# Performance work log

Measured on AMD Instinct MI355X. Metric: run time of the kernel, lower is better.

## Reference

```python
import jax, jax.numpy as jnp
import numpy as np

B, T, D, K = 8, 4096, 1024, 3


def setup_inputs() -> dict:
    key = jax.random.key(0)
    k0, k1, k2 = jax.random.split(key, 3)
    x = jax.random.normal(k0, (B, T, D), dtype=jnp.float32)
    lim = 1.0 / np.sqrt(D)
    Wv = jax.random.uniform(k1, (D, D), dtype=jnp.float32, minval=-lim, maxval=lim)
    bv = jnp.zeros((D,), dtype=jnp.float32)
    Wo = jax.random.uniform(k2, (D, D), dtype=jnp.float32, minval=-lim, maxval=lim)
    bo = jnp.zeros((D,), dtype=jnp.float32)
    neighbor_weights = jnp.ones((K,), dtype=jnp.float32) / K
    return {"x": x, "Wv": Wv, "bv": bv, "Wo": Wo, "bo": bo,
            "neighbor_weights": neighbor_weights}


def reference(x, Wv, bv, Wo, bo, neighbor_weights):
    # x: [B, T, D]; faithful translation of the unfold -> Linear -> weighted-sum chain
    k = neighbor_weights.shape[0]
    pad = k // 2
    t = x.shape[1]
    # replicate padding along T (torch F.pad mode='replicate')
    xp = jnp.pad(x, ((0, 0), (pad, pad), (0, 0)), mode='edge')  # [B, T+2*pad, D]
    # sliding windows: [B, T, K, D] (small fixed K loop, not a data-dim loop)
    windows = jnp.stack([xp[:, i:i + t, :] for i in range(k)], axis=2)
    # value projection applied per window element (nn.Linear: x @ W.T + b)
    v = jnp.einsum('btkd,ed->btke', windows, Wv) + bv  # [B, T, K, D]
    # fixed-weight neighbor average
    attended = jnp.einsum('btkd,k->btd', v, neighbor_weights)  # [B, T, D]
    # output projection
    return jnp.einsum('btd,ed->bte', attended, Wo) + bo
```

## Files before the change

kernel.cpp:

```cpp
#include <hip/hip_runtime.h>
#include <stdint.h>
#include <stddef.h>

typedef _Float16 f16_t;
typedef _Float16 f16x4 __attribute__((ext_vector_type(4)));
typedef _Float16 f16x8 __attribute__((ext_vector_type(8)));
typedef float f32x4 __attribute__((ext_vector_type(4)));

#define AS_G __attribute__((address_space(1)))
#define AS_L __attribute__((address_space(3)))

__device__ __forceinline__ void gload_lds16(const void* g, void* l) {
  __builtin_amdgcn_global_load_lds((AS_G void*)g, (AS_L void*)l, 16, 0, 0);
}

#define FENCE() asm volatile("" ::: "memory")
#define BARX()                            \
  do {                                    \
    FENCE();                              \
    __builtin_amdgcn_s_barrier();         \
    FENCE();                              \
  } while (0)
#define VMCNT(n) asm volatile("s_waitcnt vmcnt(" #n ")" ::: "memory")


__global__ __launch_bounds__(256) void prep_xavg_kernel(
    const float* __restrict__ X, const float* __restrict__ Wo,
    const float* __restrict__ Wv, const float* __restrict__ bv,
    const float* __restrict__ bo, const float* __restrict__ nw, int Kw,
    f16_t* __restrict__ Wo_h, f16_t* __restrict__ WvT, float* __restrict__ bc,
    f16_t* __restrict__ Xavg) {
  __shared__ float smem[32 * 33];
  const int b = blockIdx.x;
  const int t = threadIdx.x;
  if (b >= 3072) {
    const int T = 4096, D = 1024;
    const int base = (b - 3072) * 8;
    const int t0 = base & (T - 1);
    const int col = t * 4;
    const float w0 = nw[0], w1 = nw[1], w2 = nw[2];
    const float* xb = X + (size_t)base * D + col;
    f32x4 va = *(const f32x4*)(xb + (t0 == 0 ? 0 : -D));
    f32x4 vb = *(const f32x4*)(xb);
    f16_t* ob = Xavg + (size_t)base * D + col;
#pragma unroll
    for (int g = 0; g < 8; ++g) {
      f32x4 vc;
      if (t0 + g == T - 1) vc = vb;
      else vc = *(const f32x4*)(xb + (size_t)(g + 1) * D);
      f32x4 y = w0 * va + w1 * vb + w2 * vc;
      f16x4 o;
      o.x = (f16_t)y.x; o.y = (f16_t)y.y; o.z = (f16_t)y.z; o.w = (f16_t)y.w;
      *(f16x4*)(ob + (size_t)g * D) = o;
      va = vb;
      vb = vc;
    }
  } else if (b < 1024) {
    const int i = b * 256 + t;
    f32x4 v = ((const f32x4*)Wo)[i];
    f16x4 o;
    o.x = (f16_t)v.x; o.y = (f16_t)v.y; o.z = (f16_t)v.z; o.w = (f16_t)v.w;
    ((f16x4*)Wo_h)[i] = o;
  } else if (b < 2048) {
    const int i = b - 1024;
    const int bx = i & 31, by = i >> 5;
    const int tx = t & 31, ty = t >> 5;
#pragma unroll
    for (int k = 0; k < 32; k += 8)
      smem[(ty + k) * 33 + tx] = Wv[(size_t)(by * 32 + ty + k) * 1024 + bx * 32 + tx];
    __syncthreads();
#pragma unroll
    for (int k = 0; k < 32; k += 8)
      WvT[(size_t)(bx * 32 + ty + k) * 1024 + by * 32 + tx] = (f16_t)smem[tx * 33 + ty + k];
  } else {
    const int e = b - 2048;
    float sw = 0.f;
    for (int k = 0; k < Kw; ++k) sw += nw[k];
    float p = 0.f;
    for (int d = t; d < 1024; d += 256) p += Wo[(size_t)e * 1024 + d] * bv[d];
    smem[t] = p;
    __syncthreads();
    for (int s = 128; s > 0; s >>= 1) {
      if (t < s) smem[t] += smem[t + s];
      __syncthreads();
    }
    if (t == 0) bc[e] = sw * smem[0] + bo[e];
  }
}


template <typename OutT, bool BIAS>
__global__ __launch_bounds__(256) void gemm_bt_kernel(const f16_t* __restrict__ A,
                                                      const f16_t* __restrict__ Bt,
                                                      OutT* __restrict__ C,
                                                      const float* __restrict__ bias,
                                                      int M, int N, int K) {
  __shared__ __align__(16) f16_t sA[128 * 32];
  __shared__ __align__(16) f16_t sB[128 * 32];
  const int tid = threadIdx.x;
  const int l = tid & 63;
  const int w = tid >> 6;
  const int wr = w >> 1;
  const int wc = w & 1;
  const int nMT = M >> 7;
  const int bid = blockIdx.x;
  const int mt = bid % nMT;
  const int nt = bid / nMT;
  const int m0 = mt << 7;
  const int n0 = nt << 7;

  const int srow = (w << 4) + (l >> 2);
  const int scol = (l & 3) << 3;
  const size_t aoff0 = (size_t)(m0 + srow) * K + scol;
  const size_t boff0 = (size_t)(n0 + srow) * K + scol;
  f16_t* ldsA = sA + (w << 9);
  f16_t* ldsB = sB + (w << 9);

  f32x4 acc[4][4];
#pragma unroll
  for (int i = 0; i < 4; ++i)
#pragma unroll
    for (int j = 0; j < 4; ++j) acc[i][j] = f32x4{0.f, 0.f, 0.f, 0.f};

  const int ka = (l >> 4) << 3;
  const int ar = (wr << 6) + (l & 15);
  const int br = (wc << 6) + (l & 15);

  const int nK = K >> 5;
  for (int kt = 0; kt < nK; ++kt) {
    const int kb = kt << 5;
    gload_lds16(A + aoff0 + kb, ldsA);
    gload_lds16(A + aoff0 + ((size_t)K << 6) + kb, ldsA + 2048);
    gload_lds16(Bt + boff0 + kb, ldsB);
    gload_lds16(Bt + boff0 + ((size_t)K << 6) + kb, ldsB + 2048);
    __syncthreads();
    f16x8 af[4], bfr[4];
#pragma unroll
    for (int m = 0; m < 4; ++m) af[m] = *(const f16x8*)(sA + ((ar + (m << 4)) << 5) + ka);
#pragma unroll
    for (int n = 0; n < 4; ++n) bfr[n] = *(const f16x8*)(sB + ((br + (n << 4)) << 5) + ka);
#pragma unroll
    for (int m = 0; m < 4; ++m)
#pragma unroll
      for (int n = 0; n < 4; ++n)
        acc[m][n] = __builtin_amdgcn_mfma_f32_16x16x32_f16(af[m], bfr[n], acc[m][n], 0, 0, 0);
    __syncthreads();
  }

  const int orow = (l >> 4) << 2;
  const int ocol = l & 15;
#pragma unroll
  for (int n = 0; n < 4; ++n) {
    const int gn = n0 + (wc << 6) + (n << 4) + ocol;
    const float bs = BIAS ? bias[gn] : 0.f;
#pragma unroll
    for (int m = 0; m < 4; ++m) {
      const int gm = m0 + (wr << 6) + (m << 4) + orow;
#pragma unroll
      for (int j = 0; j < 4; ++j) {
        C[(size_t)(gm + j) * N + gn] = (OutT)(acc[m][n][j] + bs);
      }
    }
  }
}


__device__ __forceinline__ void stage256(const f16_t* __restrict__ g, int K,
                                         f16_t* ldsOp, int w, int l) {
#pragma unroll
  for (int i = 0; i < 2; ++i) {
    const int f = i * 512 + w * 64 + l;
    const int row = f >> 2;
    const int ch = f & 3;
    const int col = ((ch ^ ((row >> 1) & 3)) << 3);
    gload_lds16(g + (size_t)row * K + col, ldsOp + i * 4096 + w * 512);
  }
}

__global__ __launch_bounds__(512, 2) void gemm256_kernel(const f16_t* __restrict__ A,
                                                         const f16_t* __restrict__ Bt,
                                                         float* __restrict__ C,
                                                         const float* __restrict__ bias,
                                                         int M, int N, int K) {
  __shared__ __align__(16) f16_t lds[4 * 16384];
  const int tid = threadIdx.x;
  const int l = tid & 63;
  const int w = tid >> 6;
  const int wr = w >> 2;
  const int wc = w & 3;
  const int lr = l & 15;
  const int q = l >> 4;

  const int cpx = (int)gridDim.x >> 3;
  const int swzb = ((int)blockIdx.x & 7) * cpx + ((int)blockIdx.x >> 3);
  const int nNT = N >> 8;
  const int mt = swzb / nNT;
  const int nt = swzb % nNT;
  const int m0 = mt << 8;
  const int n0 = nt << 8;

  const f16_t* Apanel = A + (size_t)m0 * K;
  const f16_t* Bpanel = Bt + (size_t)n0 * K;
  const int sw = (q ^ ((lr >> 1) & 3)) << 3;

  f32x4 acc[8][4];
#pragma unroll
  for (int m = 0; m < 8; ++m)
#pragma unroll
    for (int n = 0; n < 4; ++n) acc[m][n] = f32x4{0.f, 0.f, 0.f, 0.f};

  const int nK = K >> 5;

  for (int t = 0; t < 3; ++t) {
    f16_t* buf = lds + (t & 3) * 16384;
    stage256(Apanel + (t << 5), K, buf, w, l);
    stage256(Bpanel + (t << 5), K, buf + 8192, w, l);
  }
  VMCNT(8);
  BARX();

  for (int t = 0; t < nK; ++t) {
    f16_t* sA = lds + (t & 3) * 16384;
    f16_t* sB = sA + 8192;

    {
      const int tn = (t + 3) < nK ? (t + 3) : (nK - 1);
      f16_t* nbuf = lds + ((t + 3) & 3) * 16384;
      stage256(Apanel + ((size_t)tn << 5), K, nbuf, w, l);
      stage256(Bpanel + ((size_t)tn << 5), K, nbuf + 8192, w, l);
    }

    f16x8 bf[4], af[4], ag[4];
#pragma unroll
    for (int n = 0; n < 4; ++n)
      bf[n] = *(const f16x8*)(sB + (((wc << 6) + (n << 4) + lr) << 5) + sw);
#pragma unroll
    for (int m = 0; m < 4; ++m)
      af[m] = *(const f16x8*)(sA + (((wr << 7) + (m << 4) + lr) << 5) + sw);
#pragma unroll
    for (int m = 0; m < 4; ++m)
      ag[m] = *(const f16x8*)(sA + (((wr << 7) + 64 + (m << 4) + lr) << 5) + sw);

    __builtin_amdgcn_s_setprio(1);
#pragma unroll
    for (int m = 0; m < 4; ++m)
#pragma unroll
      for (int n = 0; n < 4; ++n)
        acc[m][n] = __builtin_amdgcn_mfma_f32_16x16x32_f16(af[m], bf[n], acc[m][n], 0, 0, 0);
#pragma unroll
    for (int m = 0; m < 4; ++m)
#pragma unroll
      for (int n = 0; n < 4; ++n)
        acc[m + 4][n] = __builtin_amdgcn_mfma_f32_16x16x32_f16(ag[m], bf[n], acc[m + 4][n], 0, 0, 0);
    __builtin_amdgcn_s_setprio(0);

    VMCNT(8);
    BARX();
  }

  float bs[4];
#pragma unroll
  for (int n = 0; n < 4; ++n) bs[n] = bias[n0 + (wc << 6) + (n << 4) + lr];
#pragma unroll
  for (int m = 0; m < 8; ++m) {
    const int gm = m0 + (wr << 7) + (m << 4) + (q << 2);
#pragma unroll
    for (int j = 0; j < 4; ++j) {
      float* Crow = C + (size_t)(gm + j) * N + n0 + (wc << 6) + lr;
#pragma unroll
      for (int n = 0; n < 4; ++n) Crow[n << 4] = acc[m][n][j] + bs[n];
    }
  }
}


extern "C" void kernel_launch(void* const* d_in, const int* in_sizes, int n_in,
                              void* d_out, int out_size, void* d_ws, size_t ws_size,
                              hipStream_t stream) {
  const float* x = (const float*)d_in[0];
  const float* Wv = (const float*)d_in[1];
  const float* bv = (const float*)d_in[2];
  const float* Wo = (const float*)d_in[3];
  const float* bo = (const float*)d_in[4];
  const float* nw = (const float*)d_in[5];
  float* out = (float*)d_out;

  char* ws = (char*)d_ws;
  f16_t* Wo_h = (f16_t*)(ws);
  f16_t* WvT  = (f16_t*)(ws + (2u << 20));
  f16_t* WcT  = (f16_t*)(ws + (4u << 20));
  float* bc   = (float*)(ws + (6u << 20));
  f16_t* Xavg = (f16_t*)(ws + (8u << 20));

  prep_xavg_kernel<<<dim3(7168), dim3(256), 0, stream>>>(
      x, Wo, Wv, bv, bo, nw, in_sizes[5], Wo_h, WvT, bc, Xavg);
  gemm_bt_kernel<f16_t, false><<<dim3(64), dim3(256), 0, stream>>>(
      Wo_h, WvT, WcT, (const float*)nullptr, 1024, 1024, 1024);
  gemm256_kernel<<<dim3(512), dim3(512), 0, stream>>>(
      Xavg, WcT, out, bc, 32768, 1024, 1024);
}
```

Measured before the change: 146.8 us.

## Shrink main GEMM tile to 256x128 with 3-stage LDS pipeline for higher occupancy

```diff
diff --git a/kernel.cpp b/kernel.cpp
--- a/kernel.cpp
+++ b/kernel.cpp
@@ -165,24 +165,24 @@
 }
 
 
-__device__ __forceinline__ void stage256(const f16_t* __restrict__ g, int K,
-                                         f16_t* ldsOp, int w, int l) {
+__device__ __forceinline__ void stageOp(const f16_t* __restrict__ g, int K, int rows2,
+                                        f16_t* gran, int w, int l) {
 #pragma unroll
   for (int i = 0; i < 2; ++i) {
+    if (i >= rows2) break;
     const int f = i * 512 + w * 64 + l;
     const int row = f >> 2;
-    const int ch = f & 3;
-    const int col = ((ch ^ ((row >> 1) & 3)) << 3);
-    gload_lds16(g + (size_t)row * K + col, ldsOp + i * 4096 + w * 512);
-  }
-}
-
-__global__ __launch_bounds__(512, 2) void gemm256_kernel(const f16_t* __restrict__ A,
+    const int ch = (f & 3) ^ ((row >> 1) & 3);
+    gload_lds16(g + (size_t)row * K + (ch << 3), gran + i * 4096 + w * 512);
+  }
+}
+
+__global__ __launch_bounds__(512, 4) void gemm_hi_kernel(const f16_t* __restrict__ A,
                                                          const f16_t* __restrict__ Bt,
                                                          float* __restrict__ C,
                                                          const float* __restrict__ bias,
                                                          int M, int N, int K) {
-  __shared__ __align__(16) f16_t lds[4 * 16384];
+  __shared__ __align__(16) f16_t lds[3 * 12288];
   const int tid = threadIdx.x;
   const int l = tid & 63;
   const int w = tid >> 6;
@@ -193,82 +193,77 @@
 
   const int cpx = (int)gridDim.x >> 3;
   const int swzb = ((int)blockIdx.x & 7) * cpx + ((int)blockIdx.x >> 3);
-  const int nNT = N >> 8;
+  const int nNT = N >> 7;
   const int mt = swzb / nNT;
   const int nt = swzb % nNT;
   const int m0 = mt << 8;
-  const int n0 = nt << 8;
+  const int n0 = nt << 7;
 
   const f16_t* Apanel = A + (size_t)m0 * K;
   const f16_t* Bpanel = Bt + (size_t)n0 * K;
   const int sw = (q ^ ((lr >> 1) & 3)) << 3;
 
-  f32x4 acc[8][4];
+  f32x4 acc[8][2];
 #pragma unroll
   for (int m = 0; m < 8; ++m)
 #pragma unroll
-    for (int n = 0; n < 4; ++n) acc[m][n] = f32x4{0.f, 0.f, 0.f, 0.f};
+    for (int n = 0; n < 2; ++n) acc[m][n] = f32x4{0.f, 0.f, 0.f, 0.f};
 
   const int nK = K >> 5;
 
-  for (int t = 0; t < 3; ++t) {
-    f16_t* buf = lds + (t & 3) * 16384;
-    stage256(Apanel + (t << 5), K, buf, w, l);
-    stage256(Bpanel + (t << 5), K, buf + 8192, w, l);
-  }
-  VMCNT(8);
+#define STAGE(TT, GI)                                                       \
+  do {                                                                      \
+    const int ts_ = (TT) < nK ? (TT) : (nK - 1);                            \
+    f16_t* g_ = lds + (GI) * 12288;                                         \
+    stageOp(Apanel + (ts_ << 5), K, 2, g_, w, l);                           \
+    stageOp(Bpanel + (ts_ << 5), K, 1, g_ + 8192, w, l);                    \
+  } while (0)
+
+  STAGE(0, 0);
+  STAGE(1, 1);
+  VMCNT(3);
   BARX();
 
+  int cur = 0, stg = 2;
   for (int t = 0; t < nK; ++t) {
-    f16_t* sA = lds + (t & 3) * 16384;
-    f16_t* sB = sA + 8192;
-
-    {
-      const int tn = (t + 3) < nK ? (t + 3) : (nK - 1);
-      f16_t* nbuf = lds + ((t + 3) & 3) * 16384;
-      stage256(Apanel + ((size_t)tn << 5), K, nbuf, w, l);
-      stage256(Bpanel + ((size_t)tn << 5), K, nbuf + 8192, w, l);
-    }
-
-    f16x8 bf[4], af[4], ag[4];
-#pragma unroll
-    for (int n = 0; n < 4; ++n)
-      bf[n] = *(const f16x8*)(sB + (((wc << 6) + (n << 4) + lr) << 5) + sw);
-#pragma unroll
-    for (int m = 0; m < 4; ++m)
-      af[m] = *(const f16x8*)(sA + (((wr << 7) + (m << 4) + lr) << 5) + sw);
-#pragma unroll
-    for (int m = 0; m < 4; ++m)
-      ag[m] = *(const f16x8*)(sA + (((wr << 7) + 64 + (m << 4) + lr) << 5) + sw);
+    STAGE(t + 2, stg);
+
+    const f16_t* gA = lds + cur * 12288;
+    const f16_t* gB = gA + 8192;
+    f16x8 af[8], bf[2];
+#pragma unroll
+    for (int n = 0; n < 2; ++n)
+      bf[n] = *(const f16x8*)(gB + (((wc << 5) + (n << 4) + lr) << 5) + sw);
+#pragma unroll
+    for (int m = 0; m < 8; ++m)
+      af[m] = *(const f16x8*)(gA + (((wr << 7) + (m << 4) + lr) << 5) + sw);
 
     __builtin_amdgcn_s_setprio(1);
 #pragma unroll
-    for (int m = 0; m < 4; ++m)
-#pragma unroll
-      for (int n = 0; n < 4; ++n)
+    for (int m = 0; m < 8; ++m)
+#pragma unroll
+      for (int n = 0; n < 2; ++n)
         acc[m][n] = __builtin_amdgcn_mfma_f32_16x16x32_f16(af[m], bf[n], acc[m][n], 0, 0, 0);
-#pragma unroll
-    for (int m = 0; m < 4; ++m)
-#pragma unroll
-      for (int n = 0; n < 4; ++n)
-        acc[m + 4][n] = __builtin_amdgcn_mfma_f32_16x16x32_f16(ag[m], bf[n], acc[m + 4][n], 0, 0, 0);
     __builtin_amdgcn_s_setprio(0);
 
-    VMCNT(8);
+    VMCNT(3);
     BARX();
-  }
-
-  float bs[4];
-#pragma unroll
-  for (int n = 0; n < 4; ++n) bs[n] = bias[n0 + (wc << 6) + (n << 4) + lr];
+    cur = (cur == 2) ? 0 : cur + 1;
+    stg = (stg == 2) ? 0 : stg + 1;
+  }
+#undef STAGE
+
+  float bs[2];
+#pragma unroll
+  for (int n = 0; n < 2; ++n) bs[n] = bias[n0 + (wc << 5) + (n << 4) + lr];
 #pragma unroll
   for (int m = 0; m < 8; ++m) {
     const int gm = m0 + (wr << 7) + (m << 4) + (q << 2);
 #pragma unroll
     for (int j = 0; j < 4; ++j) {
-      float* Crow = C + (size_t)(gm + j) * N + n0 + (wc << 6) + lr;
-#pragma unroll
-      for (int n = 0; n < 4; ++n) Crow[n << 4] = acc[m][n][j] + bs[n];
+      float* Crow = C + (size_t)(gm + j) * N + n0 + (wc << 5) + lr;
+#pragma unroll
+      for (int n = 0; n < 2; ++n) Crow[n << 4] = acc[m][n][j] + bs[n];
     }
   }
 }
@@ -296,6 +291,6 @@
       x, Wo, Wv, bv, bo, nw, in_sizes[5], Wo_h, WvT, bc, Xavg);
   gemm_bt_kernel<f16_t, false><<<dim3(64), dim3(256), 0, stream>>>(
       Wo_h, WvT, WcT, (const float*)nullptr, 1024, 1024, 1024);
-  gemm256_kernel<<<dim3(512), dim3(512), 0, stream>>>(
+  gemm_hi_kernel<<<dim3(1024), dim3(512), 0, stream>>>(
       Xavg, WcT, out, bc, 32768, 1024, 1024);
 }
```

Result: no change. 147.7 us (+0.7%).

## Overlap X-averaging pass with the weight-combine GEMM in one launch

Applied to the files above, without the earlier changes.

```diff
diff --git a/kernel.cpp b/kernel.cpp
--- a/kernel.cpp
+++ b/kernel.cpp
@@ -24,38 +24,15 @@
 #define VMCNT(n) asm volatile("s_waitcnt vmcnt(" #n ")" ::: "memory")
 
 
-__global__ __launch_bounds__(256) void prep_xavg_kernel(
-    const float* __restrict__ X, const float* __restrict__ Wo,
-    const float* __restrict__ Wv, const float* __restrict__ bv,
-    const float* __restrict__ bo, const float* __restrict__ nw, int Kw,
-    f16_t* __restrict__ Wo_h, f16_t* __restrict__ WvT, float* __restrict__ bc,
-    f16_t* __restrict__ Xavg) {
+__global__ __launch_bounds__(256) void prep_w_kernel(
+    const float* __restrict__ Wo, const float* __restrict__ Wv,
+    const float* __restrict__ bv, const float* __restrict__ bo,
+    const float* __restrict__ nw, int Kw,
+    f16_t* __restrict__ Wo_h, f16_t* __restrict__ WvT, float* __restrict__ bc) {
   __shared__ float smem[32 * 33];
   const int b = blockIdx.x;
   const int t = threadIdx.x;
-  if (b >= 3072) {
-    const int T = 4096, D = 1024;
-    const int base = (b - 3072) * 8;
-    const int t0 = base & (T - 1);
-    const int col = t * 4;
-    const float w0 = nw[0], w1 = nw[1], w2 = nw[2];
-    const float* xb = X + (size_t)base * D + col;
-    f32x4 va = *(const f32x4*)(xb + (t0 == 0 ? 0 : -D));
-    f32x4 vb = *(const f32x4*)(xb);
-    f16_t* ob = Xavg + (size_t)base * D + col;
-#pragma unroll
-    for (int g = 0; g < 8; ++g) {
-      f32x4 vc;
-      if (t0 + g == T - 1) vc = vb;
-      else vc = *(const f32x4*)(xb + (size_t)(g + 1) * D);
-      f32x4 y = w0 * va + w1 * vb + w2 * vc;
-      f16x4 o;
-      o.x = (f16_t)y.x; o.y = (f16_t)y.y; o.z = (f16_t)y.z; o.w = (f16_t)y.w;
-      *(f16x4*)(ob + (size_t)g * D) = o;
-      va = vb;
-      vb = vc;
-    }
-  } else if (b < 1024) {
+  if (b < 1024) {
     const int i = b * 256 + t;
     f32x4 v = ((const f32x4*)Wo)[i];
     f16x4 o;
@@ -89,23 +66,49 @@
 }
 
 
-template <typename OutT, bool BIAS>
-__global__ __launch_bounds__(256) void gemm_bt_kernel(const f16_t* __restrict__ A,
-                                                      const f16_t* __restrict__ Bt,
-                                                      OutT* __restrict__ C,
-                                                      const float* __restrict__ bias,
-                                                      int M, int N, int K) {
-  __shared__ __align__(16) f16_t sA[128 * 32];
-  __shared__ __align__(16) f16_t sB[128 * 32];
+__global__ __launch_bounds__(256) void xavg_wct_kernel(
+    const float* __restrict__ X, const float* __restrict__ nw,
+    const f16_t* __restrict__ Wo_h, const f16_t* __restrict__ WvT,
+    f16_t* __restrict__ Xavg, f16_t* __restrict__ WcT) {
+  __shared__ __align__(16) f16_t smem[2 * 128 * 32];
+  const int b = blockIdx.x;
   const int tid = threadIdx.x;
+
+  if (b < 4096) {
+    const int T = 4096, D = 1024;
+    const int base = b * 8;
+    const int t0 = base & (T - 1);
+    const int col = tid * 4;
+    const float w0 = nw[0], w1 = nw[1], w2 = nw[2];
+    const float* xb = X + (size_t)base * D + col;
+    f32x4 va = *(const f32x4*)(xb + (t0 == 0 ? 0 : -D));
+    f32x4 vb = *(const f32x4*)(xb);
+    f16_t* ob = Xavg + (size_t)base * D + col;
+#pragma unroll
+    for (int g = 0; g < 8; ++g) {
+      f32x4 vc;
+      if (t0 + g == T - 1) vc = vb;
+      else vc = *(const f32x4*)(xb + (size_t)(g + 1) * D);
+      f32x4 y = w0 * va + w1 * vb + w2 * vc;
+      f16x4 o;
+      o.x = (f16_t)y.x; o.y = (f16_t)y.y; o.z = (f16_t)y.z; o.w = (f16_t)y.w;
+      *(f16x4*)(ob + (size_t)g * D) = o;
+      va = vb;
+      vb = vc;
+    }
+    return;
+  }
+
+  constexpr int K = 1024, N = 1024;
+  f16_t* sA = smem;
+  f16_t* sB = smem + 128 * 32;
   const int l = tid & 63;
   const int w = tid >> 6;
   const int wr = w >> 1;
   const int wc = w & 1;
-  const int nMT = M >> 7;
-  const int bid = blockIdx.x;
-  const int mt = bid % nMT;
-  const int nt = bid / nMT;
+  const int bid = b - 4096;
+  const int mt = bid & 7;
+  const int nt = bid >> 3;
   const int m0 = mt << 7;
   const int n0 = nt << 7;
 
@@ -126,13 +129,12 @@
   const int ar = (wr << 6) + (l & 15);
   const int br = (wc << 6) + (l & 15);
 
-  const int nK = K >> 5;
-  for (int kt = 0; kt < nK; ++kt) {
+  for (int kt = 0; kt < (K >> 5); ++kt) {
     const int kb = kt << 5;
-    gload_lds16(A + aoff0 + kb, ldsA);
-    gload_lds16(A + aoff0 + ((size_t)K << 6) + kb, ldsA + 2048);
-    gload_lds16(Bt + boff0 + kb, ldsB);
-    gload_lds16(Bt + boff0 + ((size_t)K << 6) + kb, ldsB + 2048);
+    gload_lds16(Wo_h + aoff0 + kb, ldsA);
+    gload_lds16(Wo_h + aoff0 + ((size_t)K << 6) + kb, ldsA + 2048);
+    gload_lds16(WvT + boff0 + kb, ldsB);
+    gload_lds16(WvT + boff0 + ((size_t)K << 6) + kb, ldsB + 2048);
     __syncthreads();
     f16x8 af[4], bfr[4];
 #pragma unroll
@@ -152,13 +154,12 @@
 #pragma unroll
   for (int n = 0; n < 4; ++n) {
     const int gn = n0 + (wc << 6) + (n << 4) + ocol;
-    const float bs = BIAS ? bias[gn] : 0.f;
 #pragma unroll
     for (int m = 0; m < 4; ++m) {
       const int gm = m0 + (wr << 6) + (m << 4) + orow;
 #pragma unroll
       for (int j = 0; j < 4; ++j) {
-        C[(size_t)(gm + j) * N + gn] = (OutT)(acc[m][n][j] + bs);
+        WcT[(size_t)(gm + j) * N + gn] = (f16_t)acc[m][n][j];
       }
     }
   }
@@ -172,7 +173,7 @@
     const int f = i * 512 + w * 64 + l;
     const int row = f >> 2;
     const int ch = f & 3;
-    const int col = ((ch ^ ((row >> 1) & 3)) << 3);
+    const int col = (((ch ^ ((row >> 1) & 3))) << 3);
     gload_lds16(g + (size_t)row * K + col, ldsOp + i * 4096 + w * 512);
   }
 }
@@ -292,10 +293,10 @@
   float* bc   = (float*)(ws + (6u << 20));
   f16_t* Xavg = (f16_t*)(ws + (8u << 20));
 
-  prep_xavg_kernel<<<dim3(7168), dim3(256), 0, stream>>>(
-      x, Wo, Wv, bv, bo, nw, in_sizes[5], Wo_h, WvT, bc, Xavg);
-  gemm_bt_kernel<f16_t, false><<<dim3(64), dim3(256), 0, stream>>>(
-      Wo_h, WvT, WcT, (const float*)nullptr, 1024, 1024, 1024);
+  prep_w_kernel<<<dim3(3072), dim3(256), 0, stream>>>(
+      Wo, Wv, bv, bo, nw, in_sizes[5], Wo_h, WvT, bc);
+  xavg_wct_kernel<<<dim3(4160), dim3(256), 0, stream>>>(
+      x, nw, Wo_h, WvT, Xavg, WcT);
   gemm256_kernel<<<dim3(512), dim3(512), 0, stream>>>(
       Xavg, WcT, out, bc, 32768, 1024, 1024);
 }
```

Result: no change. 145.1 us (-1.2%).

## Fuse neighbor averaging into main GEMM epilogue, reading fp32 x directly

Applied to the files above, without the earlier changes.

```diff
diff --git a/kernel.cpp b/kernel.cpp
--- a/kernel.cpp
+++ b/kernel.cpp
@@ -6,6 +6,7 @@
 typedef _Float16 f16x4 __attribute__((ext_vector_type(4)));
 typedef _Float16 f16x8 __attribute__((ext_vector_type(8)));
 typedef float f32x4 __attribute__((ext_vector_type(4)));
+typedef float f32x8 __attribute__((ext_vector_type(8)));
 
 #define AS_G __attribute__((address_space(1)))
 #define AS_L __attribute__((address_space(3)))
@@ -24,38 +25,15 @@
 #define VMCNT(n) asm volatile("s_waitcnt vmcnt(" #n ")" ::: "memory")
 
 
-__global__ __launch_bounds__(256) void prep_xavg_kernel(
-    const float* __restrict__ X, const float* __restrict__ Wo,
-    const float* __restrict__ Wv, const float* __restrict__ bv,
-    const float* __restrict__ bo, const float* __restrict__ nw, int Kw,
-    f16_t* __restrict__ Wo_h, f16_t* __restrict__ WvT, float* __restrict__ bc,
-    f16_t* __restrict__ Xavg) {
+__global__ __launch_bounds__(256) void prep_w_kernel(
+    const float* __restrict__ Wo, const float* __restrict__ Wv,
+    const float* __restrict__ bv, const float* __restrict__ bo,
+    const float* __restrict__ nw, int Kw,
+    f16_t* __restrict__ Wo_h, f16_t* __restrict__ WvT, float* __restrict__ bc) {
   __shared__ float smem[32 * 33];
   const int b = blockIdx.x;
   const int t = threadIdx.x;
-  if (b >= 3072) {
-    const int T = 4096, D = 1024;
-    const int base = (b - 3072) * 8;
-    const int t0 = base & (T - 1);
-    const int col = t * 4;
-    const float w0 = nw[0], w1 = nw[1], w2 = nw[2];
-    const float* xb = X + (size_t)base * D + col;
-    f32x4 va = *(const f32x4*)(xb + (t0 == 0 ? 0 : -D));
-    f32x4 vb = *(const f32x4*)(xb);
-    f16_t* ob = Xavg + (size_t)base * D + col;
-#pragma unroll
-    for (int g = 0; g < 8; ++g) {
-      f32x4 vc;
-      if (t0 + g == T - 1) vc = vb;
-      else vc = *(const f32x4*)(xb + (size_t)(g + 1) * D);
-      f32x4 y = w0 * va + w1 * vb + w2 * vc;
-      f16x4 o;
-      o.x = (f16_t)y.x; o.y = (f16_t)y.y; o.z = (f16_t)y.z; o.w = (f16_t)y.w;
-      *(f16x4*)(ob + (size_t)g * D) = o;
-      va = vb;
-      vb = vc;
-    }
-  } else if (b < 1024) {
+  if (b < 1024) {
     const int i = b * 256 + t;
     f32x4 v = ((const f32x4*)Wo)[i];
     f16x4 o;
@@ -165,24 +143,40 @@
 }
 
 
-__device__ __forceinline__ void stage256(const f16_t* __restrict__ g, int K,
-                                         f16_t* ldsOp, int w, int l) {
+__device__ __forceinline__ void stageA_x(const float* __restrict__ X, int m0, int bb,
+                                         int be, char* Abuf, int kt, int w, int l) {
+#pragma unroll
+  for (int i = 0; i < 5; ++i) {
+    const int f = i * 512 + w * 64 + l;
+    const int row = f >> 3;
+    const int c = f & 7;
+    int g = m0 - 32 + row;
+    g = g < bb ? bb : (g > be ? be : g);
+    const int col = (kt << 5) + (((c >> 1) ^ (row & 3)) << 3) + ((c & 1) << 2);
+    gload_lds16(X + (size_t)g * 1024 + col, Abuf + i * 8192 + w * 1024);
+  }
+}
+
+__device__ __forceinline__ void stageB_w(const f16_t* __restrict__ Bt, int n0,
+                                         char* Bgran, int kt, int w, int l) {
 #pragma unroll
   for (int i = 0; i < 2; ++i) {
     const int f = i * 512 + w * 64 + l;
     const int row = f >> 2;
-    const int ch = f & 3;
-    const int col = ((ch ^ ((row >> 1) & 3)) << 3);
-    gload_lds16(g + (size_t)row * K + col, ldsOp + i * 4096 + w * 512);
-  }
-}
-
-__global__ __launch_bounds__(512, 2) void gemm256_kernel(const f16_t* __restrict__ A,
-                                                         const f16_t* __restrict__ Bt,
-                                                         float* __restrict__ C,
-                                                         const float* __restrict__ bias,
-                                                         int M, int N, int K) {
-  __shared__ __align__(16) f16_t lds[4 * 16384];
+    const int ch = (f & 3) ^ ((row >> 1) & 3);
+    gload_lds16(Bt + (size_t)(n0 + row) * 1024 + (kt << 5) + (ch << 3),
+                Bgran + i * 8192 + w * 1024);
+  }
+}
+
+__global__ __launch_bounds__(512, 2) void gemm_fused_g_kernel(
+    const float* __restrict__ X, const f16_t* __restrict__ Bt,
+    float* __restrict__ C, const float* __restrict__ bias,
+    const float* __restrict__ nw) {
+  constexpr int N = 1024, T = 4096;
+  constexpr int nK = 32;
+  __shared__ __align__(32) char lds[131072];
+
   const int tid = threadIdx.x;
   const int l = tid & 63;
   const int w = tid >> 6;
@@ -198,77 +192,82 @@
   const int nt = swzb % nNT;
   const int m0 = mt << 8;
   const int n0 = nt << 8;
-
-  const f16_t* Apanel = A + (size_t)m0 * K;
-  const f16_t* Bpanel = Bt + (size_t)n0 * K;
-  const int sw = (q ^ ((lr >> 1) & 3)) << 3;
-
-  f32x4 acc[8][4];
-#pragma unroll
-  for (int m = 0; m < 8; ++m)
+  const int bb = (m0 >> 12) << 12;
+  const int be = bb + T - 1;
+
+  const int rowbase = (wr << 7) + 31 + lr;
+  const int axor = ((q ^ (rowbase & 3)) << 5);
+  const int bxor = ((q ^ ((lr >> 1) & 3)) << 4);
+  const int brow = (wc << 6) + lr;
+
+  f32x4 acc[9][4];
+#pragma unroll
+  for (int m = 0; m < 9; ++m)
 #pragma unroll
     for (int n = 0; n < 4; ++n) acc[m][n] = f32x4{0.f, 0.f, 0.f, 0.f};
 
-  const int nK = K >> 5;
-
-  for (int t = 0; t < 3; ++t) {
-    f16_t* buf = lds + (t & 3) * 16384;
-    stage256(Apanel + (t << 5), K, buf, w, l);
-    stage256(Bpanel + (t << 5), K, buf + 8192, w, l);
-  }
-  VMCNT(8);
+  stageA_x(X, m0, bb, be, lds, 0, w, l);
+  stageB_w(Bt, n0, lds + 81920, 0, w, l);
+  stageB_w(Bt, n0, lds + 81920 + 16384, 1, w, l);
+  VMCNT(0);
   BARX();
 
   for (int t = 0; t < nK; ++t) {
-    f16_t* sA = lds + (t & 3) * 16384;
-    f16_t* sB = sA + 8192;
-
     {
-      const int tn = (t + 3) < nK ? (t + 3) : (nK - 1);
-      f16_t* nbuf = lds + ((t + 3) & 3) * 16384;
-      stage256(Apanel + ((size_t)tn << 5), K, nbuf, w, l);
-      stage256(Bpanel + ((size_t)tn << 5), K, nbuf + 8192, w, l);
-    }
-
-    f16x8 bf[4], af[4], ag[4];
+      const int ka = (t + 1) < nK ? (t + 1) : (nK - 1);
+      stageA_x(X, m0, bb, be, lds + ((t + 1) & 1) * 40960, ka, w, l);
+      const int kb = (t + 2) < nK ? (t + 2) : (nK - 1);
+      stageB_w(Bt, n0, lds + 81920 + ((t + 2) % 3) * 16384, kb, w, l);
+    }
+
+    const char* Ac = lds + (t & 1) * 40960;
+    const char* Bc = lds + 81920 + (t % 3) * 16384;
+
+    f16x8 bf[4];
 #pragma unroll
     for (int n = 0; n < 4; ++n)
-      bf[n] = *(const f16x8*)(sB + (((wc << 6) + (n << 4) + lr) << 5) + sw);
-#pragma unroll
-    for (int m = 0; m < 4; ++m)
-      af[m] = *(const f16x8*)(sA + (((wr << 7) + (m << 4) + lr) << 5) + sw);
-#pragma unroll
-    for (int m = 0; m < 4; ++m)
-      ag[m] = *(const f16x8*)(sA + (((wr << 7) + 64 + (m << 4) + lr) << 5) + sw);
+      bf[n] = *(const f16x8*)(Bc + ((brow + (n << 4)) << 6) + bxor);
 
     __builtin_amdgcn_s_setprio(1);
 #pragma unroll
-    for (int m = 0; m < 4; ++m)
+    for (int m = 0; m < 9; ++m) {
+      f32x8 av = *(const f32x8*)(Ac + ((rowbase + (m << 4)) << 7) + axor);
+      f16x8 am;
+#pragma unroll
+      for (int e = 0; e < 8; ++e) am[e] = (f16_t)av[e];
 #pragma unroll
       for (int n = 0; n < 4; ++n)
-        acc[m][n] = __builtin_amdgcn_mfma_f32_16x16x32_f16(af[m], bf[n], acc[m][n], 0, 0, 0);
-#pragma unroll
-    for (int m = 0; m < 4; ++m)
-#pragma unroll
-      for (int n = 0; n < 4; ++n)
-        acc[m + 4][n] = __builtin_amdgcn_mfma_f32_16x16x32_f16(ag[m], bf[n], acc[m + 4][n], 0, 0, 0);
+        acc[m][n] = __builtin_amdgcn_mfma_f32_16x16x32_f16(am, bf[n], acc[m][n], 0, 0, 0);
+    }
     __builtin_amdgcn_s_setprio(0);
 
-    VMCNT(8);
+    VMCNT(2);
     BARX();
   }
 
+  const float w0 = nw[0], w1 = nw[1], w2 = nw[2];
+  const int lswap = (l + 16) & 63;
   float bs[4];
 #pragma unroll
   for (int n = 0; n < 4; ++n) bs[n] = bias[n0 + (wc << 6) + (n << 4) + lr];
+
 #pragma unroll
   for (int m = 0; m < 8; ++m) {
     const int gm = m0 + (wr << 7) + (m << 4) + (q << 2);
 #pragma unroll
-    for (int j = 0; j < 4; ++j) {
-      float* Crow = C + (size_t)(gm + j) * N + n0 + (wc << 6) + lr;
-#pragma unroll
-      for (int n = 0; n < 4; ++n) Crow[n << 4] = acc[m][n][j] + bs[n];
+    for (int n = 0; n < 4; ++n) {
+      const float sel0 = (q == 0) ? acc[m + 1][n][0] : acc[m][n][0];
+      const float sel1 = (q == 0) ? acc[m + 1][n][1] : acc[m][n][1];
+      const float s0 = __shfl(sel0, lswap, 64);
+      const float s1 = __shfl(sel1, lswap, 64);
+      const float a0 = acc[m][n][0], a1 = acc[m][n][1];
+      const float a2 = acc[m][n][2], a3 = acc[m][n][3];
+      const int gn = n0 + (wc << 6) + (n << 4) + lr;
+      float* Ccol = C + (size_t)gm * N + gn;
+      Ccol[0]            = w0 * a0 + w1 * a1 + w2 * a2 + bs[n];
+      Ccol[(size_t)N]    = w0 * a1 + w1 * a2 + w2 * a3 + bs[n];
+      Ccol[(size_t)N*2]  = w0 * a2 + w1 * a3 + w2 * s0 + bs[n];
+      Ccol[(size_t)N*3]  = w0 * a3 + w1 * s0 + w2 * s1 + bs[n];
     }
   }
 }
@@ -290,12 +289,11 @@
   f16_t* WvT  = (f16_t*)(ws + (2u << 20));
   f16_t* WcT  = (f16_t*)(ws + (4u << 20));
   float* bc   = (float*)(ws + (6u << 20));
-  f16_t* Xavg = (f16_t*)(ws + (8u << 20));
-
-  prep_xavg_kernel<<<dim3(7168), dim3(256), 0, stream>>>(
-      x, Wo, Wv, bv, bo, nw, in_sizes[5], Wo_h, WvT, bc, Xavg);
+
+  prep_w_kernel<<<dim3(3072), dim3(256), 0, stream>>>(
+      Wo, Wv, bv, bo, nw, in_sizes[5], Wo_h, WvT, bc);
   gemm_bt_kernel<f16_t, false><<<dim3(64), dim3(256), 0, stream>>>(
       Wo_h, WvT, WcT, (const float*)nullptr, 1024, 1024, 1024);
-  gemm256_kernel<<<dim3(512), dim3(512), 0, stream>>>(
-      Xavg, WcT, out, bc, 32768, 1024, 1024);
-}
+  gemm_fused_g_kernel<<<dim3(512), dim3(512), 0, stream>>>(
+      x, WcT, out, bc, nw);
+}
```

Result: slower. 177.4 us (+20.9%).
